# Optimization experiments

Hardware: AMD Instinct MI355X
Metric: run time of the kernel (lower is better)

Reference implementation:

```python
import jax, jax.numpy as jnp
import numpy as np
from jax import lax

B, HW, PS, MP, ED, NH = 32, 256, 16, 20, 64, 4


def _conv(x, w, b):
    y = lax.conv_general_dilated(x, w, (1, 1), 'SAME', dimension_numbers=('NCHW', 'OIHW', 'NCHW'))
    return y + b[None, :, None, None]


def _maxpool2(x):
    return lax.reduce_window(x, -jnp.inf, lax.max, (1, 1, 2, 2), (1, 1, 2, 2), 'VALID')


def _extract(x, c1w, c1b, c2w, c2b, c3w, c3b, c4w, c4b, fcw, fcb):
    # FeatureExtractor: conv-conv-pool, conv-conv-pool, adaptive avg pool (4,4), fc -> 128
    x = x[:, None]  # (B,1,H,W)
    x = jax.nn.relu(_conv(x, c1w, c1b))
    x = jax.nn.relu(_conv(x, c2w, c2b))
    x = _maxpool2(x)
    x = jax.nn.relu(_conv(x, c3w, c3b))
    x = jax.nn.relu(_conv(x, c4w, c4b))
    x = _maxpool2(x)
    b_, c_, h_, w_ = x.shape
    x = x.reshape(b_, c_, 4, h_ // 4, 4, w_ // 4).mean((3, 5))  # AdaptiveAvgPool2d((4,4))
    return x.reshape(b_, -1) @ fcw.T + fcb


def _rope(x):
    # x: (B, heads, S, D); faithful to RotaryPositionalEmbedding (identity at S=1)
    S, D = x.shape[-2], x.shape[-1]
    pos = jnp.arange(S, dtype=jnp.float32)[:, None]
    freqs = jnp.exp(jnp.arange(0, D, 2, dtype=jnp.float32) * (-np.log(10000.0) / D))
    emb = pos * freqs  # (S, D/2)
    cos = jnp.cos(emb)[None, :, None, :]
    sin = jnp.sin(emb)[None, :, None, :]
    x1, x2 = jnp.split(x, 2, axis=-1)
    return jnp.concatenate([x1 * cos - x2 * sin, x1 * sin + x2 * cos], -1)


def _attn(x, wq, wk, wv, wow, wob):
    b_, s_, d_ = x.shape
    hd = d_ // NH
    scale = hd ** -0.5
    def heads(w):
        return (x @ w.T).reshape(b_, s_, NH, hd).transpose(0, 2, 1, 3)
    q, k, v = heads(wq), heads(wk), heads(wv)
    q, k = _rope(q), _rope(k)
    a = jax.nn.softmax(jnp.einsum('bhqd,bhkd->bhqk', q, k) * scale, -1)
    o = jnp.einsum('bhqk,bhkd->bhqd', a, v).transpose(0, 2, 1, 3).reshape(b_, s_, d_)
    return o @ wow.T + wob


def _patch_feats(sig, pew, peb):
    # SignalPatching: row-major stride-8 16x16 patches, first MP=20, embed, mean over patches
    H, W = sig.shape[1], sig.shape[2]
    stride = PS // 2
    pos = [(i, j) for i in range(0, H - PS + 1, stride) for j in range(0, W - PS + 1, stride)][:MP]
    ri = np.array([p[0] for p in pos])[:, None] + np.arange(PS)  # (MP,PS)
    ci = np.array([p[1] for p in pos])[:, None] + np.arange(PS)
    patches = sig[:, ri[:, :, None], ci[:, None, :]]  # (B,MP,PS,PS)
    emb = patches.reshape(sig.shape[0], len(pos), PS * PS) @ pew.T + peb  # (B,MP,ED)
    return emb.mean(1)


def _forward(time_input, freq_input,
             t_c1w, t_c1b, t_c2w, t_c2b, t_c3w, t_c3b, t_c4w, t_c4b, t_fcw, t_fcb,
             t_redw, t_redb, t_wq, t_wk, t_wv, t_wow, t_wob, t_pew, t_peb,
             f_c1w, f_c1b, f_c2w, f_c2b, f_c3w, f_c3b, f_c4w, f_c4b, f_fcw, f_fcb,
             f_redw, f_redb, f_wq, f_wk, f_wv, f_wow, f_wob, f_pew, f_peb,
             c1w, c1b, c2w, c2b, c3w, c3b):
    tf = _extract(time_input, t_c1w, t_c1b, t_c2w, t_c2b, t_c3w, t_c3b, t_c4w, t_c4b, t_fcw, t_fcb)
    tp = _patch_feats(time_input, t_pew, t_peb)
    tr = jax.nn.relu(tf @ t_redw.T + t_redb)  # DimensionalityReducer (eval: dropout off)
    ta = _attn(tr[:, None, :], t_wq, t_wk, t_wv, t_wow, t_wob)[:, 0]
    ff = _extract(freq_input, f_c1w, f_c1b, f_c2w, f_c2b, f_c3w, f_c3b, f_c4w, f_c4b, f_fcw, f_fcb)
    fp = _patch_feats(freq_input, f_pew, f_peb)
    fr = jax.nn.relu(ff @ f_redw.T + f_redb)
    fa = _attn(fr[:, None, :], f_wq, f_wk, f_wv, f_wow, f_wob)[:, 0]
    feats = jnp.concatenate([ta, fa, tp, fp], -1)  # (B, 256)
    h = jax.nn.relu(feats @ c1w.T + c1b)
    h = jax.nn.relu(h @ c2w.T + c2b)
    return h @ c3w.T + c3b  # (B, num_classes)


def setup_inputs() -> dict:
    key = jax.random.key(0)
    ks = iter(jax.random.split(key, 64))
    def nrm(*shape):
        return jax.random.normal(next(ks), shape, jnp.float32) * 0.05
    d = {
        'time_input': jax.random.normal(next(ks), (B, HW, HW), jnp.float32),
        'freq_input': jax.random.normal(next(ks), (B, HW, HW), jnp.float32),
    }
    for p in ('t', 'f'):
        d[p + '_c1w'] = nrm(32, 1, 3, 3); d[p + '_c1b'] = jnp.zeros(32, jnp.float32)
        d[p + '_c2w'] = nrm(32, 32, 3, 3); d[p + '_c2b'] = jnp.zeros(32, jnp.float32)
        d[p + '_c3w'] = nrm(64, 32, 3, 3); d[p + '_c3b'] = jnp.zeros(64, jnp.float32)
        d[p + '_c4w'] = nrm(64, 64, 3, 3); d[p + '_c4b'] = jnp.zeros(64, jnp.float32)
        d[p + '_fcw'] = nrm(128, 64 * 4 * 4); d[p + '_fcb'] = jnp.zeros(128, jnp.float32)
        d[p + '_redw'] = nrm(64, 128); d[p + '_redb'] = jnp.zeros(64, jnp.float32)
        d[p + '_wq'] = nrm(64, 64); d[p + '_wk'] = nrm(64, 64); d[p + '_wv'] = nrm(64, 64)
        d[p + '_wow'] = nrm(64, 64); d[p + '_wob'] = jnp.zeros(64, jnp.float32)
        d[p + '_pew'] = nrm(ED, PS * PS); d[p + '_peb'] = jnp.zeros(ED, jnp.float32)
    d['c1w'] = nrm(256, 256); d['c1b'] = jnp.zeros(256, jnp.float32)
    d['c2w'] = nrm(128, 256); d['c2b'] = jnp.zeros(128, jnp.float32)
    d['c3w'] = nrm(2, 128); d['c3b'] = jnp.zeros(2, jnp.float32)
    return d


def reference(time_input, freq_input,
              t_c1w, t_c1b, t_c2w, t_c2b, t_c3w, t_c3b, t_c4w, t_c4b, t_fcw, t_fcb,
              t_redw, t_redb, t_wq, t_wk, t_wv, t_wow, t_wob, t_pew, t_peb,
              f_c1w, f_c1b, f_c2w, f_c2b, f_c3w, f_c3b, f_c4w, f_c4b, f_fcw, f_fcb,
              f_redw, f_redb, f_wq, f_wk, f_wv, f_wow, f_wob, f_pew, f_peb,
              c1w, c1b, c2w, c2b, c3w, c3b):
    return _forward(time_input, freq_input,
                    t_c1w, t_c1b, t_c2w, t_c2b, t_c3w, t_c3b, t_c4w, t_c4b, t_fcw, t_fcb,
                    t_redw, t_redb, t_wq, t_wk, t_wv, t_wow, t_wob, t_pew, t_peb,
                    f_c1w, f_c1b, f_c2w, f_c2b, f_c3w, f_c3b, f_c4w, f_c4b, f_fcw, f_fcb,
                    f_redw, f_redb, f_wq, f_wk, f_wv, f_wow, f_wob, f_pew, f_peb,
                    c1w, c1b, c2w, c2b, c3w, c3b)
```

## Files before the change

### kernel.cpp

```cpp
#include <hip/hip_runtime.h>


typedef short bf16x8 __attribute__((ext_vector_type(8)));
typedef float f32x4 __attribute__((ext_vector_type(4)));

__device__ __forceinline__ unsigned short bf16_rne(float f) {
    unsigned int u = __float_as_uint(f);
    u += 0x7fffu + ((u >> 16) & 1u);
    return (unsigned short)(u >> 16);
}
__device__ __forceinline__ float bf2f(unsigned short h) {
    unsigned int u = ((unsigned int)h) << 16;
    return __uint_as_float(u);
}

template <int CIN, int COUT>
__global__ void wcvt_kernel(const float* __restrict__ w, unsigned short* __restrict__ wq) {
    int idx = blockIdx.x * 256 + threadIdx.x;
    if (idx >= COUT * CIN * 9) return;
    int ci  = idx & 31;
    int co  = (idx >> 5) & 31;
    int kk  = (idx >> 10) % 9;
    int t   = (idx >> 10) / 9;
    int cc  = t % (CIN / 32);
    int cot = t / (CIN / 32);
    float f = w[((size_t)(cot * 32 + co) * CIN + cc * 32 + ci) * 9 + kk];
    wq[idx] = bf16_rne(f);
}

__global__ void conv1_nhwc_kernel(const float* __restrict__ in, const float* __restrict__ w,
                                  const float* __restrict__ bias, unsigned short* __restrict__ out) {
    __shared__ float xr[3][72];
    __shared__ float ws[288];
    __shared__ float bs[32];
    int x0  = blockIdx.x * 64;
    int y   = blockIdx.y;
    int img = blockIdx.z;
    int tid = threadIdx.x;
    for (int idx = tid; idx < 288; idx += 256) ws[idx] = w[idx];
    if (tid < 32) bs[tid] = bias[tid];
    for (int idx = tid; idx < 3 * 66; idx += 256) {
        int r = idx / 66, c = idx % 66;
        int gy = y - 1 + r, gx = x0 - 1 + c;
        xr[r][c] = (gy >= 0 && gy < 256 && gx >= 0 && gx < 256)
                       ? in[(size_t)img * 65536 + gy * 256 + gx] : 0.f;
    }
    __syncthreads();
    int co = tid & 31, lx = tid >> 5;
    float wk[9];
    #pragma unroll
    for (int k = 0; k < 9; ++k) wk[k] = ws[co * 9 + k];
    float bb = bs[co];
    #pragma unroll
    for (int s = 0; s < 8; ++s) {
        int xl = 8 * s + lx;
        float acc = bb;
        #pragma unroll
        for (int ky = 0; ky < 3; ++ky) {
            #pragma unroll
            for (int kx = 0; kx < 3; ++kx) acc = fmaf(wk[ky * 3 + kx], xr[ky][xl + kx], acc);
        }
        out[(((size_t)img * 256 + y) * 256 + (x0 + xl)) * 32 + co] = bf16_rne(fmaxf(acc, 0.f));
    }
}

template <int CIN, int COUT, int H, bool POOL>
__global__ __launch_bounds__(256, 3) void convmfma_kernel(const unsigned short* __restrict__ in,
                                                          const unsigned short* __restrict__ wq,
                                                          const float* __restrict__ bias,
                                                          unsigned short* __restrict__ out) {
    constexpr int COT = COUT / 32;
    __shared__ __align__(16) unsigned short xls[10][34][40];
    __shared__ __align__(16) unsigned short wsh[9][32][40];
    int x0  = blockIdx.x * 32;
    int y0  = blockIdx.y * 8;
    int img = blockIdx.z / COT;
    int cot = blockIdx.z % COT;
    int tid  = threadIdx.x;
    int lane = tid & 63, wvi = tid >> 6;
    int l15 = lane & 15, q8 = (lane >> 4) << 3;

    f32x4 acc[2][2][2];
    #pragma unroll
    for (int a = 0; a < 2; ++a)
        #pragma unroll
        for (int b = 0; b < 2; ++b)
            #pragma unroll
            for (int c = 0; c < 2; ++c) acc[a][b][c] = (f32x4){0.f, 0.f, 0.f, 0.f};

    const unsigned short* inI = in + (size_t)img * H * H * CIN;

    for (int cc = 0; cc < CIN / 32; ++cc) {
        if (cc) __syncthreads();
        for (int idx = tid; idx < 10 * 34 * 4; idx += 256) {
            int row = idx / 136, rem = idx % 136, xx = rem >> 2, c4 = rem & 3;
            int gy = y0 - 1 + row, gx = x0 - 1 + xx;
            uint4 v = {0u, 0u, 0u, 0u};
            if (gy >= 0 && gy < H && gx >= 0 && gx < H)
                v = *(const uint4*)&inI[((size_t)gy * H + gx) * CIN + cc * 32 + c4 * 8];
            *(uint4*)&xls[row][xx][c4 * 8] = v;
        }
        const unsigned short* wsrc = wq + (size_t)(cot * (CIN / 32) + cc) * 9216;
        #pragma unroll
        for (int it = 0; it < 5; ++it) {
            int idx = tid + it * 256;
            if (idx < 1152) {
                int kk = idx >> 7;
                int r  = idx & 127;
                int co = r >> 2, c4 = r & 3;
                *(uint4*)&wsh[kk][co][c4 * 8] = *(const uint4*)&wsrc[idx * 8];
            }
        }
        __syncthreads();

        #pragma unroll
        for (int kk = 0; kk < 9; ++kk) {
            int ky = kk / 3, kx = kk - ky * 3;
            bf16x8 b0 = *(const bf16x8*)&wsh[kk][l15][q8];
            bf16x8 b1 = *(const bf16x8*)&wsh[kk][16 + l15][q8];
            #pragma unroll
            for (int yr = 0; yr < 2; ++yr) {
                int row = 2 * wvi + yr + ky;
                #pragma unroll
                for (int mf = 0; mf < 2; ++mf) {
                    bf16x8 a = *(const bf16x8*)&xls[row][mf * 16 + l15 + kx][q8];
                    acc[yr][mf][0] = __builtin_amdgcn_mfma_f32_16x16x32_bf16(a, b0, acc[yr][mf][0], 0, 0, 0);
                    acc[yr][mf][1] = __builtin_amdgcn_mfma_f32_16x16x32_bf16(a, b1, acc[yr][mf][1], 0, 0, 0);
                }
            }
        }
    }

    float bv[2] = {bias[cot * 32 + l15], bias[cot * 32 + 16 + l15]};
    if constexpr (POOL) {
        constexpr int Wp = H / 2;
        int yp = y0 / 2 + wvi;
        #pragma unroll
        for (int nf = 0; nf < 2; ++nf) {
            int co = cot * 32 + nf * 16 + l15;
            #pragma unroll
            for (int mf = 0; mf < 2; ++mf) {
                #pragma unroll
                for (int t = 0; t < 2; ++t) {
                    float m = fmaxf(fmaxf(acc[0][mf][nf][2 * t], acc[0][mf][nf][2 * t + 1]),
                                    fmaxf(acc[1][mf][nf][2 * t], acc[1][mf][nf][2 * t + 1]));
                    m = fmaxf(m + bv[nf], 0.f);
                    int xp = x0 / 2 + mf * 8 + 2 * (lane >> 4) + t;
                    out[(((size_t)img * Wp + yp) * Wp + xp) * COUT + co] = bf16_rne(m);
                }
            }
        }
    } else {
        #pragma unroll
        for (int yr = 0; yr < 2; ++yr) {
            int y = y0 + 2 * wvi + yr;
            #pragma unroll
            for (int mf = 0; mf < 2; ++mf) {
                #pragma unroll
                for (int nf = 0; nf < 2; ++nf) {
                    int co = cot * 32 + nf * 16 + l15;
                    #pragma unroll
                    for (int r = 0; r < 4; ++r) {
                        int x = x0 + mf * 16 + 4 * (lane >> 4) + r;
                        out[(((size_t)img * H + y) * H + x) * COUT + co] =
                            bf16_rne(fmaxf(acc[yr][mf][nf][r] + bv[nf], 0.f));
                    }
                }
            }
        }
    }
}

__global__ void avgfc_kernel(const unsigned short* __restrict__ pin, const float* __restrict__ fcw,
                             const float* __restrict__ fcb, float* __restrict__ tf) {
    __shared__ float av[1024];
    int b = blockIdx.x, tid = threadIdx.x;
    const unsigned short* p = pin + (size_t)b * 64 * 64 * 64;
    for (int idx = tid; idx < 1024; idx += 256) {
        int c = idx & 63, pq = idx >> 6, i = pq >> 2, j = pq & 3;
        float s = 0.f;
        for (int r = 0; r < 16; ++r)
            for (int cc2 = 0; cc2 < 16; ++cc2)
                s += bf2f(p[(((size_t)(i * 16 + r) * 64) + (j * 16 + cc2)) * 64 + c]);
        av[c * 16 + pq] = s * (1.f / 256.f);
    }
    __syncthreads();
    if (tid < 128) {
        float s         = fcb[tid];
        const float* wr = fcw + (size_t)tid * 1024;
        for (int i = 0; i < 1024; ++i) s = fmaf(av[i], wr[i], s);
        tf[b * 128 + tid] = s;
    }
}

__global__ void patch_kernel(const float* __restrict__ sig, const float* __restrict__ pew,
                             const float* __restrict__ peb, float* __restrict__ tp) {
    __shared__ float ps[16][168];
    __shared__ float partial[4][64];
    int b   = blockIdx.x;
    int tid = threadIdx.x;
    for (int idx = tid; idx < 16 * 168; idx += 256) {
        int r = idx / 168, c = idx % 168;
        ps[r][c] = sig[(size_t)b * 65536 + r * 256 + c];
    }
    __syncthreads();
    int e = tid & 63, pg = tid >> 6;
    const float* wr = pew + (size_t)e * 256;
    float s = 0.f;
    for (int r = 0; r < 16; ++r) {
        #pragma unroll
        for (int c = 0; c < 16; ++c) {
            float acc = 0.f;
            for (int pi = pg; pi < 20; pi += 4) acc += ps[r][8 * pi + c];
            s = fmaf(acc, wr[r * 16 + c], s);
        }
    }
    partial[pg][e] = s;
    __syncthreads();
    if (tid < 64) {
        tp[b * 64 + tid] =
            (partial[0][tid] + partial[1][tid] + partial[2][tid] + partial[3][tid]) * (1.f / 20.f) +
            peb[tid];
    }
}

__global__ void redattn_kernel(const float* __restrict__ tf, const float* __restrict__ redw,
                               const float* __restrict__ redb, const float* __restrict__ wv,
                               const float* __restrict__ wow, const float* __restrict__ wob,
                               float* __restrict__ ta) {
    __shared__ float stf[128], str_[64], sv[64];
    int b = blockIdx.x, t = threadIdx.x;
    stf[t]      = tf[b * 128 + t];
    stf[t + 64] = tf[b * 128 + 64 + t];
    __syncthreads();
    float s = redb[t];
    for (int i = 0; i < 128; ++i) s = fmaf(stf[i], redw[t * 128 + i], s);
    str_[t] = fmaxf(s, 0.f);
    __syncthreads();
    s = 0.f;
    for (int i = 0; i < 64; ++i) s = fmaf(str_[i], wv[t * 64 + i], s);
    sv[t] = s;
    __syncthreads();
    s = wob[t];
    for (int i = 0; i < 64; ++i) s = fmaf(sv[i], wow[t * 64 + i], s);
    ta[b * 64 + t] = s;
}

__global__ void head_kernel(const float* __restrict__ taT, const float* __restrict__ taF,
                            const float* __restrict__ tpT, const float* __restrict__ tpF,
                            const float* __restrict__ c1w, const float* __restrict__ c1b,
                            const float* __restrict__ c2w, const float* __restrict__ c2b,
                            const float* __restrict__ c3w, const float* __restrict__ c3b,
                            float* __restrict__ outp) {
    __shared__ float f0[256], h1[256], h2[128];
    int b = blockIdx.x, t = threadIdx.x;
    int seg = t >> 6, e = t & 63;
    const float* sp_ = (seg == 0) ? taT : (seg == 1) ? taF : (seg == 2) ? tpT : tpF;
    f0[t] = sp_[b * 64 + e];
    __syncthreads();
    {
        float s = c1b[t];
        for (int i = 0; i < 256; ++i) s = fmaf(f0[i], c1w[t * 256 + i], s);
        h1[t] = fmaxf(s, 0.f);
    }
    __syncthreads();
    if (t < 128) {
        float s = c2b[t];
        for (int i = 0; i < 256; ++i) s = fmaf(h1[i], c2w[t * 256 + i], s);
        h2[t] = fmaxf(s, 0.f);
    }
    __syncthreads();
    if (t < 2) {
        float s = c3b[t];
        for (int i = 0; i < 128; ++i) s = fmaf(h2[i], c3w[t * 128 + i], s);
        outp[b * 2 + t] = s;
    }
}

extern "C" void kernel_launch(void* const* d_in, const int* in_sizes, int n_in,
                              void* d_out, int out_size, void* d_ws, size_t ws_size,
                              hipStream_t stream) {
    constexpr size_t A_PER = 2097152, B_PER = 524288;
    constexpr size_t SMALL_BYTES = 65536 + 262144;

    int CH = 32;
    while (CH > 1 && ((size_t)CH * (A_PER + B_PER) * 2 + SMALL_BYTES) > ws_size) CH >>= 1;
    const int NCHUNK = 32 / CH;

    unsigned short* A  = (unsigned short*)d_ws;
    unsigned short* Bb = A + (size_t)CH * A_PER;
    float* SM = (float*)(Bb + (size_t)CH * B_PER);
    float* tfB[2] = {SM, SM + 4096};
    float* tpB[2] = {SM + 8192, SM + 10240};
    float* taB[2] = {SM + 12288, SM + 14336};
    unsigned short* WQ = (unsigned short*)(SM + 16384);

    for (int br = 0; br < 2; ++br) {
        const float* in   = (const float*)d_in[br];
        const int base    = 2 + br * 19;
        const float* c1w  = (const float*)d_in[base + 0];
        const float* c1b  = (const float*)d_in[base + 1];
        const float* c2w  = (const float*)d_in[base + 2];
        const float* c2b  = (const float*)d_in[base + 3];
        const float* c3w  = (const float*)d_in[base + 4];
        const float* c3b  = (const float*)d_in[base + 5];
        const float* c4w  = (const float*)d_in[base + 6];
        const float* c4b  = (const float*)d_in[base + 7];
        const float* fcw  = (const float*)d_in[base + 8];
        const float* fcb  = (const float*)d_in[base + 9];
        const float* redw = (const float*)d_in[base + 10];
        const float* redb = (const float*)d_in[base + 11];
        const float* wv_  = (const float*)d_in[base + 14];
        const float* wow_ = (const float*)d_in[base + 15];
        const float* wob_ = (const float*)d_in[base + 16];
        const float* pew  = (const float*)d_in[base + 17];
        const float* peb  = (const float*)d_in[base + 18];

        unsigned short* wq2 = WQ + (size_t)br * 64512;
        unsigned short* wq3 = wq2 + 9216;
        unsigned short* wq4 = wq3 + 18432;
        wcvt_kernel<32, 32><<<36, 256, 0, stream>>>(c2w, wq2);
        wcvt_kernel<32, 64><<<72, 256, 0, stream>>>(c3w, wq3);
        wcvt_kernel<64, 64><<<144, 256, 0, stream>>>(c4w, wq4);

        for (int ck = 0; ck < NCHUNK; ++ck) {
            const float* inC = in + (size_t)ck * CH * 65536;
            conv1_nhwc_kernel<<<dim3(4, 256, CH), 256, 0, stream>>>(inC, c1w, c1b, A);
            convmfma_kernel<32, 32, 256, true>
                <<<dim3(8, 32, CH), 256, 0, stream>>>(A, wq2, c2b, Bb);
            convmfma_kernel<32, 64, 128, false>
                <<<dim3(4, 16, CH * 2), 256, 0, stream>>>(Bb, wq3, c3b, A);
            convmfma_kernel<64, 64, 128, true>
                <<<dim3(4, 16, CH * 2), 256, 0, stream>>>(A, wq4, c4b, Bb);
            avgfc_kernel<<<CH, 256, 0, stream>>>(Bb, fcw, fcb, tfB[br] + (size_t)ck * CH * 128);
            patch_kernel<<<CH, 256, 0, stream>>>(inC, pew, peb, tpB[br] + (size_t)ck * CH * 64);
        }
        redattn_kernel<<<32, 64, 0, stream>>>(tfB[br], redw, redb, wv_, wow_, wob_, taB[br]);
    }

    head_kernel<<<32, 256, 0, stream>>>(taB[0], taB[1], tpB[0], tpB[1],
                                        (const float*)d_in[40], (const float*)d_in[41],
                                        (const float*)d_in[42], (const float*)d_in[43],
                                        (const float*)d_in[44], (const float*)d_in[45],
                                        (float*)d_out);
}
```

Measured before the change: 804.1 us.

## Compute all output channels per block and read weights directly from global

The MFMA conv kernel now computes every output channel in one block instead of splitting COUT across grid z, so the input halo tile is staged in LDS once per image instead of once per 32-channel group. Weight fragments are no longer staged in shared memory and are loaded straight from global/L2 in a new COUT-major packed layout, with wcvt rewritten to match. Launch-bounds occupancy targets become per-instantiation template values. In exchange, the larger accumulator arrays raise register pressure, and the weight loads go through global memory inside the inner loop, which can add latency.

```diff
diff --git a/kernel.cpp b/kernel.cpp
--- a/kernel.cpp
+++ b/kernel.cpp
@@ -18,14 +18,12 @@
 __global__ void wcvt_kernel(const float* __restrict__ w, unsigned short* __restrict__ wq) {
     int idx = blockIdx.x * 256 + threadIdx.x;
     if (idx >= COUT * CIN * 9) return;
-    int ci  = idx & 31;
-    int co  = (idx >> 5) & 31;
-    int kk  = (idx >> 10) % 9;
-    int t   = (idx >> 10) / 9;
-    int cc  = t % (CIN / 32);
-    int cot = t / (CIN / 32);
-    float f = w[((size_t)(cot * 32 + co) * CIN + cc * 32 + ci) * 9 + kk];
-    wq[idx] = bf16_rne(f);
+    int ci = idx & 31;
+    int co = (idx >> 5) % COUT;
+    int r  = (idx >> 5) / COUT;
+    int kk = r % 9;
+    int cc = r / 9;
+    wq[idx] = bf16_rne(w[((size_t)co * CIN + cc * 32 + ci) * 9 + kk]);
 }
 
 __global__ void conv1_nhwc_kernel(const float* __restrict__ in, const float* __restrict__ w,
@@ -64,29 +62,27 @@
     }
 }
 
-template <int CIN, int COUT, int H, bool POOL>
-__global__ __launch_bounds__(256, 3) void convmfma_kernel(const unsigned short* __restrict__ in,
-                                                          const unsigned short* __restrict__ wq,
-                                                          const float* __restrict__ bias,
-                                                          unsigned short* __restrict__ out) {
-    constexpr int COT = COUT / 32;
+template <int CIN, int COUT, int H, bool POOL, int MINW>
+__global__ __launch_bounds__(256, MINW) void convmfma_kernel(const unsigned short* __restrict__ in,
+                                                             const unsigned short* __restrict__ wq,
+                                                             const float* __restrict__ bias,
+                                                             unsigned short* __restrict__ out) {
+    constexpr int NF = COUT / 16;
     __shared__ __align__(16) unsigned short xls[10][34][40];
-    __shared__ __align__(16) unsigned short wsh[9][32][40];
     int x0  = blockIdx.x * 32;
     int y0  = blockIdx.y * 8;
-    int img = blockIdx.z / COT;
-    int cot = blockIdx.z % COT;
+    int img = blockIdx.z;
     int tid  = threadIdx.x;
     int lane = tid & 63, wvi = tid >> 6;
     int l15 = lane & 15, q8 = (lane >> 4) << 3;
 
-    f32x4 acc[2][2][2];
+    f32x4 acc[2][2][NF];
     #pragma unroll
     for (int a = 0; a < 2; ++a)
         #pragma unroll
         for (int b = 0; b < 2; ++b)
             #pragma unroll
-            for (int c = 0; c < 2; ++c) acc[a][b][c] = (f32x4){0.f, 0.f, 0.f, 0.f};
+            for (int c = 0; c < NF; ++c) acc[a][b][c] = (f32x4){0.f, 0.f, 0.f, 0.f};
 
     const unsigned short* inI = in + (size_t)img * H * H * CIN;
 
@@ -100,44 +96,41 @@
                 v = *(const uint4*)&inI[((size_t)gy * H + gx) * CIN + cc * 32 + c4 * 8];
             *(uint4*)&xls[row][xx][c4 * 8] = v;
         }
-        const unsigned short* wsrc = wq + (size_t)(cot * (CIN / 32) + cc) * 9216;
-        #pragma unroll
-        for (int it = 0; it < 5; ++it) {
-            int idx = tid + it * 256;
-            if (idx < 1152) {
-                int kk = idx >> 7;
-                int r  = idx & 127;
-                int co = r >> 2, c4 = r & 3;
-                *(uint4*)&wsh[kk][co][c4 * 8] = *(const uint4*)&wsrc[idx * 8];
-            }
-        }
         __syncthreads();
 
+        const unsigned short* wqc = wq + (size_t)cc * 9 * COUT * 32;
         #pragma unroll
         for (int kk = 0; kk < 9; ++kk) {
             int ky = kk / 3, kx = kk - ky * 3;
-            bf16x8 b0 = *(const bf16x8*)&wsh[kk][l15][q8];
-            bf16x8 b1 = *(const bf16x8*)&wsh[kk][16 + l15][q8];
+            bf16x8 bfr[NF];
+            #pragma unroll
+            for (int nf = 0; nf < NF; ++nf)
+                bfr[nf] = *(const bf16x8*)&wqc[((size_t)kk * COUT + nf * 16 + l15) * 32 + q8];
             #pragma unroll
             for (int yr = 0; yr < 2; ++yr) {
                 int row = 2 * wvi + yr + ky;
                 #pragma unroll
                 for (int mf = 0; mf < 2; ++mf) {
                     bf16x8 a = *(const bf16x8*)&xls[row][mf * 16 + l15 + kx][q8];
-                    acc[yr][mf][0] = __builtin_amdgcn_mfma_f32_16x16x32_bf16(a, b0, acc[yr][mf][0], 0, 0, 0);
-                    acc[yr][mf][1] = __builtin_amdgcn_mfma_f32_16x16x32_bf16(a, b1, acc[yr][mf][1], 0, 0, 0);
+                    #pragma unroll
+                    for (int nf = 0; nf < NF; ++nf)
+                        acc[yr][mf][nf] =
+                            __builtin_amdgcn_mfma_f32_16x16x32_bf16(a, bfr[nf], acc[yr][mf][nf], 0, 0, 0);
                 }
             }
         }
     }
 
-    float bv[2] = {bias[cot * 32 + l15], bias[cot * 32 + 16 + l15]};
+    float bv[NF];
+    #pragma unroll
+    for (int nf = 0; nf < NF; ++nf) bv[nf] = bias[nf * 16 + l15];
+
     if constexpr (POOL) {
         constexpr int Wp = H / 2;
         int yp = y0 / 2 + wvi;
         #pragma unroll
-        for (int nf = 0; nf < 2; ++nf) {
-            int co = cot * 32 + nf * 16 + l15;
+        for (int nf = 0; nf < NF; ++nf) {
+            int co = nf * 16 + l15;
             #pragma unroll
             for (int mf = 0; mf < 2; ++mf) {
                 #pragma unroll
@@ -157,8 +150,8 @@
             #pragma unroll
             for (int mf = 0; mf < 2; ++mf) {
                 #pragma unroll
-                for (int nf = 0; nf < 2; ++nf) {
-                    int co = cot * 32 + nf * 16 + l15;
+                for (int nf = 0; nf < NF; ++nf) {
+                    int co = nf * 16 + l15;
                     #pragma unroll
                     for (int r = 0; r < 4; ++r) {
                         int x = x0 + mf * 16 + 4 * (lane >> 4) + r;
@@ -326,12 +319,12 @@
         for (int ck = 0; ck < NCHUNK; ++ck) {
             const float* inC = in + (size_t)ck * CH * 65536;
             conv1_nhwc_kernel<<<dim3(4, 256, CH), 256, 0, stream>>>(inC, c1w, c1b, A);
-            convmfma_kernel<32, 32, 256, true>
+            convmfma_kernel<32, 32, 256, true, 5>
                 <<<dim3(8, 32, CH), 256, 0, stream>>>(A, wq2, c2b, Bb);
-            convmfma_kernel<32, 64, 128, false>
-                <<<dim3(4, 16, CH * 2), 256, 0, stream>>>(Bb, wq3, c3b, A);
-            convmfma_kernel<64, 64, 128, true>
-                <<<dim3(4, 16, CH * 2), 256, 0, stream>>>(A, wq4, c4b, Bb);
+            convmfma_kernel<32, 64, 128, false, 4>
+                <<<dim3(4, 16, CH), 256, 0, stream>>>(Bb, wq3, c3b, A);
+            convmfma_kernel<64, 64, 128, true, 4>
+                <<<dim3(4, 16, CH), 256, 0, stream>>>(A, wq4, c4b, Bb);
             avgfc_kernel<<<CH, 256, 0, stream>>>(Bb, fcw, fcb, tfB[br] + (size_t)ck * CH * 128);
             patch_kernel<<<CH, 256, 0, stream>>>(inC, pew, peb, tpB[br] + (size_t)ck * CH * 64);
         }
```

Result: slower. 888.0 us (+10.4%).
